# Kernel optimization log

Hardware: AMD Instinct MI355X
Metric: run time of the kernel (lower is better)

## Reference

```python
import jax, jax.numpy as jnp
import numpy as np

N = 100000   # nodes
E = 1600000  # edges
IN, HID, OUT = 128, 128, 64

def setup_inputs() -> dict:
    key = jax.random.key(0)
    ks = jax.random.split(key, 18)
    def lin(k, i, o):
        kw, kb = jax.random.split(k)
        s = 1.0 / np.sqrt(i)
        return (jax.random.uniform(kw, (i, o), jnp.float32, -s, s),
                jax.random.uniform(kb, (o,), jnp.float32, -s, s))
    x = jax.random.normal(ks[0], (N, IN), jnp.float32)
    edge_index = jax.random.randint(ks[1], (2, E), 0, N, jnp.int64)
    W1, b1   = lin(ks[2], IN, HID)
    W21, b21 = lin(ks[3], IN, HID)
    W22, b22 = lin(ks[4], HID, HID)
    W31, b31 = lin(ks[5], IN, HID)
    W32, b32 = lin(ks[6], HID, HID)
    W33, b33 = lin(ks[7], HID, HID)
    Wa, ba   = lin(ks[8], HID, 1)
    Wf, bf   = lin(ks[9], HID, OUT)
    return dict(x=x, edge_index=edge_index, W1=W1, b1=b1, W21=W21, b21=b21,
                W22=W22, b22=b22, W31=W31, b31=b31, W32=W32, b32=b32,
                W33=W33, b33=b33, Wa=Wa, ba=ba, Wf=Wf, bf=bf)

def _gcn(x, W, b, src, dst, dinv):
    # PyG GCNConv: D^{-1/2}(A+I)D^{-1/2} X W + b, self-loops added.
    h = x @ W                                    # [N, F]
    norm = dinv[src] * dinv[dst]                 # [E]
    agg = jax.ops.segment_sum(h[src] * norm[:, None], dst, num_segments=N)
    agg = agg + h * (dinv * dinv)[:, None]       # self-loop contribution
    return agg + b

def reference(x, edge_index, W1, b1, W21, b21, W22, b22, W31, b31,
              W32, b32, W33, b33, Wa, ba, Wf, bf):
    src, dst = edge_index[0], edge_index[1]
    # degree with self-loops (in-degree at target nodes)
    deg = jax.ops.segment_sum(jnp.ones(E, x.dtype), dst, num_segments=N) + 1.0
    dinv = jax.lax.rsqrt(deg)
    h1 = jax.nn.relu(_gcn(x, W1, b1, src, dst, dinv))
    h2 = jax.nn.relu(_gcn(x, W21, b21, src, dst, dinv))
    h2 = jax.nn.relu(_gcn(h2, W22, b22, src, dst, dinv))
    h3 = jax.nn.relu(_gcn(x, W31, b31, src, dst, dinv))
    h3 = jax.nn.relu(_gcn(h3, W32, b32, src, dst, dinv))
    h3 = jax.nn.relu(_gcn(h3, W33, b33, src, dst, dinv))
    H = jnp.stack([h1, h2, h3], axis=1)          # [N, 3, HID]
    scores = H @ Wa + ba                         # [N, 3, 1]
    w = jax.nn.softmax(scores, axis=1)
    h_meta = jnp.sum(w * H, axis=1)              # [N, HID]
    h_out = h_meta + h1
    return h_out @ Wf + bf                       # [N, OUT]
```

## Files before the change

### kernel.cpp

```cpp
#include <hip/hip_runtime.h>
#include <hip/hip_bf16.h>

#define HIDF 128
#define OUTF 64
#define SCAN_B 256

typedef __attribute__((ext_vector_type(8))) short bf16x8;
typedef __attribute__((ext_vector_type(4))) float f32x4;

__device__ __forceinline__ float us2f(unsigned u_lo16) {
    return __uint_as_float(u_lo16 << 16);
}
__device__ __forceinline__ unsigned short f2us(float f) {
    __hip_bfloat16 h = __float2bfloat16(f);
    return *reinterpret_cast<unsigned short*>(&h);
}
__device__ __forceinline__ unsigned pack2(float a, float b) {
    return (unsigned)f2us(a) | ((unsigned)f2us(b) << 16);
}

__global__ __launch_bounds__(256) void deg_zero(int* __restrict__ d, int N) {
    int i = blockIdx.x * 256 + threadIdx.x;
    if (i < N) d[i] = 0;
}

__global__ __launch_bounds__(256) void deg_count(const int* __restrict__ ei, int* __restrict__ d, int E) {
    int e = blockIdx.x * 256 + threadIdx.x;
    if (e < E) atomicAdd(&d[ei[E + e]], 1);
}

__global__ __launch_bounds__(256) void scanA(const int* __restrict__ degi, int* __restrict__ blocksum, int N) {
    __shared__ int red[256];
    const int b = blockIdx.x;
    const int chunk = (N + SCAN_B - 1) / SCAN_B;
    const int lo = b * chunk, hi = min(lo + chunk, N);
    int s = 0;
    for (int i = lo + threadIdx.x; i < hi; i += 256) s += degi[i];
    red[threadIdx.x] = s;
    __syncthreads();
    for (int off = 128; off; off >>= 1) {
        if (threadIdx.x < off) red[threadIdx.x] += red[threadIdx.x + off];
        __syncthreads();
    }
    if (threadIdx.x == 0) blocksum[b] = red[0];
}

__global__ __launch_bounds__(256) void scanB(const int* __restrict__ blocksum, int* __restrict__ blockoff) {
    __shared__ int ps[256];
    const int t = threadIdx.x;
    ps[t] = blocksum[t];
    __syncthreads();
    for (int off = 1; off < 256; off <<= 1) {
        int v = ps[t];
        int u = (t >= off) ? ps[t - off] : 0;
        __syncthreads();
        ps[t] = v + u;
        __syncthreads();
    }
    blockoff[t] = (t == 0) ? 0 : ps[t - 1];
}

__global__ __launch_bounds__(256) void scanC(const int* __restrict__ degi,
                                             const int* __restrict__ blockoff,
                                             int* __restrict__ cursor,
                                             float* __restrict__ dinv, int N) {
    __shared__ int ps[256];
    const int b = blockIdx.x;
    const int chunk = (N + SCAN_B - 1) / SCAN_B;
    const int lo = b * chunk, hi = min(lo + chunk, N);
    const int tchunk = (chunk + 255) / 256;
    const int tlo = lo + threadIdx.x * tchunk;
    const int thi = min(tlo + tchunk, hi);
    int s = 0;
    for (int i = tlo; i < thi; ++i) s += degi[i];
    ps[threadIdx.x] = s;
    __syncthreads();
    for (int off = 1; off < 256; off <<= 1) {
        int v = ps[threadIdx.x];
        int u = (threadIdx.x >= off) ? ps[threadIdx.x - off] : 0;
        __syncthreads();
        ps[threadIdx.x] = v + u;
        __syncthreads();
    }
    int base = blockoff[b] + ((threadIdx.x == 0) ? 0 : ps[threadIdx.x - 1]);
    for (int i = tlo; i < thi; ++i) {
        int d = degi[i];
        cursor[i] = base;
        base += d;
        dinv[i] = rsqrtf((float)d + 1.f);
    }
}

__global__ __launch_bounds__(256) void scatter_kernel(const int* __restrict__ ei,
                                                      int* __restrict__ cursor,
                                                      int* __restrict__ csr_src, int E) {
    int e = blockIdx.x * 256 + threadIdx.x;
    if (e >= E) return;
    int pos = atomicAdd(&cursor[ei[E + e]], 1);
    csr_src[pos] = ei[e];
}

__global__ __launch_bounds__(256) void cvt_scale(const float* __restrict__ X,
                                                 const float* __restrict__ dinv,
                                                 unsigned short* __restrict__ TB, int N) {
    int g = blockIdx.x * 256 + threadIdx.x;
    if (g >= N * 32) return;
    int n = g >> 5;
    float dv = dinv[n];
    float4 v = ((const float4*)X)[g];
    ushort4 o;
    o.x = f2us(v.x * dv); o.y = f2us(v.y * dv);
    o.z = f2us(v.z * dv); o.w = f2us(v.w * dv);
    ((ushort4*)TB)[g] = o;
}

__global__ __launch_bounds__(256) void cvt_w(const float* __restrict__ Wa0,
                                             const float* __restrict__ Wa1,
                                             const float* __restrict__ Wa2,
                                             const float* __restrict__ Wa3,
                                             const float* __restrict__ Wa4,
                                             unsigned short* __restrict__ WTB) {
    int t = blockIdx.x * 256 + threadIdx.x;
    if (t >= 5 * 16384) return;
    int m = t >> 14, local = t & 16383;
    int n = local >> 7, k = local & 127;
    const float* src = (m == 0) ? Wa0 : (m == 1) ? Wa1 : (m == 2) ? Wa2 : (m == 3) ? Wa3 : Wa4;
    WTB[t] = f2us(src[k * 128 + n]);
}

template <bool OUT_BF16>
__global__ __launch_bounds__(256) void agg_b(const unsigned short* __restrict__ TB,
                                             const float* __restrict__ dinv,
                                             const int* __restrict__ csr_src,
                                             const int* __restrict__ rend,
                                             void* __restrict__ O, int N) {
    const int n = (blockIdx.x * 256 + threadIdx.x) >> 6;
    const int lane = threadIdx.x & 63;
    if (n >= N) return;
    const int start = (n == 0) ? 0 : rend[n - 1];
    const int end   = rend[n];
    const unsigned* Tv = (const unsigned*)TB;

    float ax0 = 0.f, ay0 = 0.f, ax1 = 0.f, ay1 = 0.f;
    int e = start;
    for (; e + 8 <= end; e += 8) {
        int s0 = csr_src[e + 0], s1 = csr_src[e + 1], s2 = csr_src[e + 2], s3 = csr_src[e + 3];
        int s4 = csr_src[e + 4], s5 = csr_src[e + 5], s6 = csr_src[e + 6], s7 = csr_src[e + 7];
        unsigned v0 = Tv[(size_t)s0 * 64 + lane];
        unsigned v1 = Tv[(size_t)s1 * 64 + lane];
        unsigned v2 = Tv[(size_t)s2 * 64 + lane];
        unsigned v3 = Tv[(size_t)s3 * 64 + lane];
        unsigned v4 = Tv[(size_t)s4 * 64 + lane];
        unsigned v5 = Tv[(size_t)s5 * 64 + lane];
        unsigned v6 = Tv[(size_t)s6 * 64 + lane];
        unsigned v7 = Tv[(size_t)s7 * 64 + lane];
        ax0 += us2f(v0 & 0xffffu); ay0 += __uint_as_float(v0 & 0xffff0000u);
        ax1 += us2f(v1 & 0xffffu); ay1 += __uint_as_float(v1 & 0xffff0000u);
        ax0 += us2f(v2 & 0xffffu); ay0 += __uint_as_float(v2 & 0xffff0000u);
        ax1 += us2f(v3 & 0xffffu); ay1 += __uint_as_float(v3 & 0xffff0000u);
        ax0 += us2f(v4 & 0xffffu); ay0 += __uint_as_float(v4 & 0xffff0000u);
        ax1 += us2f(v5 & 0xffffu); ay1 += __uint_as_float(v5 & 0xffff0000u);
        ax0 += us2f(v6 & 0xffffu); ay0 += __uint_as_float(v6 & 0xffff0000u);
        ax1 += us2f(v7 & 0xffffu); ay1 += __uint_as_float(v7 & 0xffff0000u);
    }
    if (e + 4 <= end) {
        int s0 = csr_src[e + 0], s1 = csr_src[e + 1], s2 = csr_src[e + 2], s3 = csr_src[e + 3];
        unsigned v0 = Tv[(size_t)s0 * 64 + lane];
        unsigned v1 = Tv[(size_t)s1 * 64 + lane];
        unsigned v2 = Tv[(size_t)s2 * 64 + lane];
        unsigned v3 = Tv[(size_t)s3 * 64 + lane];
        ax0 += us2f(v0 & 0xffffu); ay0 += __uint_as_float(v0 & 0xffff0000u);
        ax1 += us2f(v1 & 0xffffu); ay1 += __uint_as_float(v1 & 0xffff0000u);
        ax0 += us2f(v2 & 0xffffu); ay0 += __uint_as_float(v2 & 0xffff0000u);
        ax1 += us2f(v3 & 0xffffu); ay1 += __uint_as_float(v3 & 0xffff0000u);
        e += 4;
    }
    for (; e < end; ++e) {
        int s = csr_src[e];
        unsigned v = Tv[(size_t)s * 64 + lane];
        ax0 += us2f(v & 0xffffu);
        ay0 += __uint_as_float(v & 0xffff0000u);
    }
    unsigned sv = Tv[(size_t)n * 64 + lane];
    ax0 += us2f(sv & 0xffffu);
    ay0 += __uint_as_float(sv & 0xffff0000u);
    const float dv = dinv[n];
    float ox = (ax0 + ax1) * dv;
    float oy = (ay0 + ay1) * dv;
    if (OUT_BF16) {
        ((unsigned*)O)[(size_t)n * 64 + lane] = pack2(ox, oy);
    } else {
        float2 o; o.x = ox; o.y = oy;
        ((float2*)O)[(size_t)n * 64 + lane] = o;
    }
}

__global__ __launch_bounds__(256) void agg_dual(const unsigned short* __restrict__ TB23,
                                                const float* __restrict__ dinv,
                                                const int* __restrict__ csr_src,
                                                const int* __restrict__ rend,
                                                unsigned* __restrict__ OA,
                                                unsigned* __restrict__ OB, int N) {
    const int n = (blockIdx.x * 256 + threadIdx.x) >> 6;
    const int lane = threadIdx.x & 63;
    if (n >= N) return;
    const int start = (n == 0) ? 0 : rend[n - 1];
    const int end   = rend[n];
    const unsigned* Tv = (const unsigned*)TB23;

    float ax2 = 0.f, ay2 = 0.f, bx2 = 0.f, by2 = 0.f;
    float ax3 = 0.f, ay3 = 0.f, bx3 = 0.f, by3 = 0.f;
    int e = start;
    for (; e + 4 <= end; e += 4) {
        int s0 = csr_src[e + 0], s1 = csr_src[e + 1], s2 = csr_src[e + 2], s3 = csr_src[e + 3];
        unsigned a0 = Tv[(size_t)s0 * 128 + lane];
        unsigned c0 = Tv[(size_t)s0 * 128 + 64 + lane];
        unsigned a1 = Tv[(size_t)s1 * 128 + lane];
        unsigned c1 = Tv[(size_t)s1 * 128 + 64 + lane];
        unsigned a2 = Tv[(size_t)s2 * 128 + lane];
        unsigned c2 = Tv[(size_t)s2 * 128 + 64 + lane];
        unsigned a3 = Tv[(size_t)s3 * 128 + lane];
        unsigned c3 = Tv[(size_t)s3 * 128 + 64 + lane];
        ax2 += us2f(a0 & 0xffffu); ay2 += __uint_as_float(a0 & 0xffff0000u);
        ax3 += us2f(c0 & 0xffffu); ay3 += __uint_as_float(c0 & 0xffff0000u);
        bx2 += us2f(a1 & 0xffffu); by2 += __uint_as_float(a1 & 0xffff0000u);
        bx3 += us2f(c1 & 0xffffu); by3 += __uint_as_float(c1 & 0xffff0000u);
        ax2 += us2f(a2 & 0xffffu); ay2 += __uint_as_float(a2 & 0xffff0000u);
        ax3 += us2f(c2 & 0xffffu); ay3 += __uint_as_float(c2 & 0xffff0000u);
        bx2 += us2f(a3 & 0xffffu); by2 += __uint_as_float(a3 & 0xffff0000u);
        bx3 += us2f(c3 & 0xffffu); by3 += __uint_as_float(c3 & 0xffff0000u);
    }
    for (; e < end; ++e) {
        int s = csr_src[e];
        unsigned a = Tv[(size_t)s * 128 + lane];
        unsigned c = Tv[(size_t)s * 128 + 64 + lane];
        ax2 += us2f(a & 0xffffu); ay2 += __uint_as_float(a & 0xffff0000u);
        ax3 += us2f(c & 0xffffu); ay3 += __uint_as_float(c & 0xffff0000u);
    }
    {
        unsigned a = Tv[(size_t)n * 128 + lane];
        unsigned c = Tv[(size_t)n * 128 + 64 + lane];
        ax2 += us2f(a & 0xffffu); ay2 += __uint_as_float(a & 0xffff0000u);
        ax3 += us2f(c & 0xffffu); ay3 += __uint_as_float(c & 0xffff0000u);
    }
    const float dv = dinv[n];
    OA[(size_t)n * 64 + lane] = pack2((ax2 + bx2) * dv, (ay2 + by2) * dv);
    OB[(size_t)n * 64 + lane] = pack2((ax3 + bx3) * dv, (ay3 + by3) * dv);
}

#define OM_BF16 1
#define OM_BF16_SR 2
template <int OMODE, int OSTRIDE, bool INF32>
__global__ __launch_bounds__(256) void gemm_mfma(const void* __restrict__ Xv,
                                                 const unsigned short* __restrict__ WT,
                                                 const float* __restrict__ bias,
                                                 const float* __restrict__ dinv,
                                                 unsigned short* __restrict__ T, int N) {
    __shared__ unsigned short Xs[64 * 128];
    __shared__ unsigned short Ws[128 * 128];
    const int tid = threadIdx.x;
    const int nb = blockIdx.x * 64;

    for (int c = tid; c < 2048; c += 256) {
        int n = c >> 4, kc = c & 15;
        ((uint4*)Ws)[(n << 4) | (kc ^ (n & 7))] = ((const uint4*)WT)[c];
    }
    for (int c = tid; c < 1024; c += 256) {
        int nl = c >> 4, kc = c & 15;
        int n = nb + nl;
        uint4 v = make_uint4(0u, 0u, 0u, 0u);
        if (n < N) {
            if (INF32) {
                const float4* Xr = (const float4*)((const float*)Xv + (size_t)n * HIDF);
                float4 v0 = Xr[kc * 2], v1 = Xr[kc * 2 + 1];
                v.x = pack2(v0.x, v0.y); v.y = pack2(v0.z, v0.w);
                v.z = pack2(v1.x, v1.y); v.w = pack2(v1.z, v1.w);
            } else {
                v = ((const uint4*)((const unsigned short*)Xv + (size_t)n * HIDF))[kc];
            }
        }
        ((uint4*)Xs)[(nl << 4) | (kc ^ (nl & 7))] = v;
    }
    __syncthreads();

    const int wv   = tid >> 6;
    const int l    = tid & 63;
    const int row  = l & 15;
    const int kgrp = l >> 4;

    bf16x8 afr[4];
    #pragma unroll
    for (int kk = 0; kk < 4; ++kk) {
        int nl = 16 * wv + row;
        int kc = kk * 4 + kgrp;
        afr[kk] = *(const bf16x8*)(Xs + nl * 128 + ((kc ^ (nl & 7)) << 3));
    }

    f32x4 acc[8];
    #pragma unroll
    for (int nt = 0; nt < 8; ++nt) {
        float b = bias[nt * 16 + row];
        acc[nt] = (f32x4){b, b, b, b};
    }

    #pragma unroll
    for (int nt = 0; nt < 8; ++nt) {
        int col = nt * 16 + row;
        #pragma unroll
        for (int kk = 0; kk < 4; ++kk) {
            int kc = kk * 4 + kgrp;
            bf16x8 bfr = *(const bf16x8*)(Ws + col * 128 + ((kc ^ (col & 7)) << 3));
            acc[nt] = __builtin_amdgcn_mfma_f32_16x16x32_bf16(afr[kk], bfr, acc[nt], 0, 0, 0);
        }
    }

    float dv[4];
    if (OMODE == OM_BF16_SR) {
        #pragma unroll
        for (int r = 0; r < 4; ++r) {
            int grow = nb + 16 * wv + kgrp * 4 + r;
            dv[r] = (grow < N) ? dinv[grow] : 0.f;
        }
    }
    #pragma unroll
    for (int nt = 0; nt < 8; ++nt) {
        int gcol = nt * 16 + row;
        #pragma unroll
        for (int r = 0; r < 4; ++r) {
            int grow = nb + 16 * wv + kgrp * 4 + r;
            if (grow < N) {
                float v = acc[nt][r];
                if (OMODE == OM_BF16_SR) v = fmaxf(v, 0.f) * dv[r];
                T[(size_t)grow * OSTRIDE + gcol] = f2us(v);
            }
        }
    }
}

__global__ __launch_bounds__(256) void gemm128f(const float* __restrict__ X,
                                                const float* __restrict__ W,
                                                const float* __restrict__ bias,
                                                float* __restrict__ T, int N) {
    __shared__ float Xsh[HIDF][68];
    const int tid = threadIdx.x;
    const int nb = blockIdx.x * 64;
    {
        const int nloc = tid & 63;
        const int n = nb + nloc;
        const int kq0 = tid >> 6;
        if (n < N) {
            const float4* Xr = (const float4*)(X + (size_t)n * HIDF);
            #pragma unroll
            for (int kq = kq0; kq < 32; kq += 4) {
                float4 v = Xr[kq];
                int k = kq * 4;
                Xsh[k + 0][nloc] = v.x; Xsh[k + 1][nloc] = v.y;
                Xsh[k + 2][nloc] = v.z; Xsh[k + 3][nloc] = v.w;
            }
        } else {
            #pragma unroll
            for (int kq = kq0; kq < 32; kq += 4) {
                int k = kq * 4;
                Xsh[k + 0][nloc] = 0.f; Xsh[k + 1][nloc] = 0.f;
                Xsh[k + 2][nloc] = 0.f; Xsh[k + 3][nloc] = 0.f;
            }
        }
    }
    __syncthreads();

    const int j4  = tid & 31;
    const int sub = tid >> 5;
    const float4* Wrow = (const float4*)W;
    const float4 bv = ((const float4*)bias)[j4];

    float4 acc[8];
    #pragma unroll
    for (int i = 0; i < 8; ++i) acc[i] = bv;

    #pragma unroll 4
    for (int k = 0; k < HIDF; ++k) {
        float4 w = Wrow[k * 32 + j4];
        float xv[8];
        *(float4*)&xv[0] = *(const float4*)&Xsh[k][sub * 8];
        *(float4*)&xv[4] = *(const float4*)&Xsh[k][sub * 8 + 4];
        #pragma unroll
        for (int i = 0; i < 8; ++i) {
            acc[i].x = fmaf(xv[i], w.x, acc[i].x);
            acc[i].y = fmaf(xv[i], w.y, acc[i].y);
            acc[i].z = fmaf(xv[i], w.z, acc[i].z);
            acc[i].w = fmaf(xv[i], w.w, acc[i].w);
        }
    }
    #pragma unroll
    for (int i = 0; i < 8; ++i) {
        int n = nb + sub * 8 + i;
        if (n < N) *((float4*)&T[(size_t)n * HIDF + j4 * 4]) = acc[i];
    }
}

__global__ __launch_bounds__(256) void meta_kernel(const float* __restrict__ H1,
                                                   const unsigned short* __restrict__ H2B,
                                                   const unsigned short* __restrict__ H3B,
                                                   const float* __restrict__ Wa,
                                                   const float* __restrict__ ba,
                                                   const float* __restrict__ Wf,
                                                   const float* __restrict__ bfb,
                                                   float* __restrict__ out, int N) {
    __shared__ float WfS[HIDF * OUTF];
    __shared__ float WaS[HIDF];
    __shared__ float hm[4][HIDF];
    const int tid = threadIdx.x;
    for (int i = tid; i < HIDF * OUTF; i += 256) WfS[i] = Wf[i];
    if (tid < HIDF) WaS[tid] = Wa[tid];
    __syncthreads();
    const float bav = ba[0];
    const int w = tid >> 6;
    const int l = tid & 63;
    const float bfv = bfb[l];
    const int iters = (N + 3) >> 2;

    for (int it = blockIdx.x; it < iters; it += gridDim.x) {
        const int n = it * 4 + w;
        __syncthreads();
        if (n < N) {
            const float* h1 = H1 + (size_t)n * HIDF;
            const unsigned short* h2 = H2B + (size_t)n * HIDF;
            const unsigned short* h3 = H3B + (size_t)n * HIDF;
            float h1a = fmaxf(h1[l], 0.f),       h1b = fmaxf(h1[l + 64], 0.f);
            float h2a = fmaxf(us2f(h2[l]), 0.f), h2b = fmaxf(us2f(h2[l + 64]), 0.f);
            float h3a = fmaxf(us2f(h3[l]), 0.f), h3b = fmaxf(us2f(h3[l + 64]), 0.f);
            float s1 = h1a * WaS[l] + h1b * WaS[l + 64];
            float s2 = h2a * WaS[l] + h2b * WaS[l + 64];
            float s3 = h3a * WaS[l] + h3b * WaS[l + 64];
            #pragma unroll
            for (int off = 32; off; off >>= 1) {
                s1 += __shfl_xor(s1, off);
                s2 += __shfl_xor(s2, off);
                s3 += __shfl_xor(s3, off);
            }
            s1 += bav; s2 += bav; s3 += bav;
            float m  = fmaxf(s1, fmaxf(s2, s3));
            float e1 = expf(s1 - m), e2 = expf(s2 - m), e3 = expf(s3 - m);
            float inv = 1.f / (e1 + e2 + e3);
            float w1 = e1 * inv, w2 = e2 * inv, w3 = e3 * inv;
            hm[w][l]      = w1 * h1a + w2 * h2a + w3 * h3a + h1a;
            hm[w][l + 64] = w1 * h1b + w2 * h2b + w3 * h3b + h1b;
        }
        __syncthreads();
        if (n < N) {
            float acc = bfv;
            #pragma unroll
            for (int k = 0; k < HIDF; ++k) acc = fmaf(hm[w][k], WfS[k * OUTF + l], acc);
            out[(size_t)n * OUTF + l] = acc;
        }
    }
}

extern "C" void kernel_launch(void* const* d_in, const int* in_sizes, int n_in,
                              void* d_out, int out_size, void* d_ws, size_t ws_size,
                              hipStream_t stream) {
    const float* x   = (const float*)d_in[0];
    const int*   ei  = (const int*)d_in[1];
    const float *W1  = (const float*)d_in[2],  *b1  = (const float*)d_in[3];
    const float *W21 = (const float*)d_in[4],  *b21 = (const float*)d_in[5];
    const float *W22 = (const float*)d_in[6],  *b22 = (const float*)d_in[7];
    const float *W31 = (const float*)d_in[8],  *b31 = (const float*)d_in[9];
    const float *W32 = (const float*)d_in[10], *b32 = (const float*)d_in[11];
    const float *W33 = (const float*)d_in[12], *b33 = (const float*)d_in[13];
    const float *Wa  = (const float*)d_in[14], *ba  = (const float*)d_in[15];
    const float *Wf  = (const float*)d_in[16], *bfb = (const float*)d_in[17];

    const int N = in_sizes[0] / HIDF;
    const int E = in_sizes[1] / 2;

    int*   DEGI    = (int*)d_ws;
    int*   CURSOR  = DEGI + N;
    int*   CSR_SRC = CURSOR + N;
    int*   BSUM    = CSR_SRC + E;
    int*   BOFF    = BSUM + 256;
    float* DINV    = (float*)(BOFF + 256);
    unsigned short* TB23 = (unsigned short*)(DINV + N);
    float* PX      = (float*)(TB23 + (size_t)N * 256);
    unsigned* AGA  = (unsigned*)(PX + (size_t)N * HIDF);
    unsigned* AGB  = AGA + (size_t)N * 64;
    unsigned* H2B  = AGB + (size_t)N * 64;
    unsigned short* WTB = (unsigned short*)(H2B + (size_t)N * 64);

    const int gN    = (N + 255) / 256;
    const int gE    = (E + 255) / 256;
    const int gCVT  = (N * 32 + 255) / 256;
    const int gAGG  = (N * 64 + 255) / 256;
    const int gGEMM = (N + 63) / 64;
    const int gMETA = 2048;

    deg_zero<<<gN, 256, 0, stream>>>(DEGI, N);
    deg_count<<<gE, 256, 0, stream>>>(ei, DEGI, E);
    scanA<<<SCAN_B, 256, 0, stream>>>(DEGI, BSUM, N);
    scanB<<<1, 256, 0, stream>>>(BSUM, BOFF);
    scanC<<<SCAN_B, 256, 0, stream>>>(DEGI, BOFF, CURSOR, DINV, N);
    scatter_kernel<<<gE, 256, 0, stream>>>(ei, CURSOR, CSR_SRC, E);
    cvt_w<<<320, 256, 0, stream>>>(W21, W31, W22, W32, W33, WTB);

    unsigned short* TBX = TB23;

    cvt_scale<<<gCVT, 256, 0, stream>>>(x, DINV, TBX, N);
    agg_b<false><<<gAGG, 256, 0, stream>>>(TBX, DINV, CSR_SRC, CURSOR, PX, N);

    gemm_mfma<OM_BF16_SR, 256, true><<<gGEMM, 256, 0, stream>>>(PX, WTB,           b21, DINV, TB23,       N);
    gemm_mfma<OM_BF16_SR, 256, true><<<gGEMM, 256, 0, stream>>>(PX, WTB + 16384,   b31, DINV, TB23 + 128, N);
    agg_dual<<<gAGG, 256, 0, stream>>>(TB23, DINV, CSR_SRC, CURSOR, AGA, AGB, N);

    gemm_mfma<OM_BF16, 128, false><<<gGEMM, 256, 0, stream>>>(AGA, WTB + 2 * 16384, b22, DINV, (unsigned short*)H2B, N);
    gemm_mfma<OM_BF16_SR, 128, false><<<gGEMM, 256, 0, stream>>>(AGB, WTB + 3 * 16384, b32, DINV, TBX, N);
    agg_b<true><<<gAGG, 256, 0, stream>>>(TBX, DINV, CSR_SRC, CURSOR, AGA, N);
    gemm_mfma<OM_BF16, 128, false><<<gGEMM, 256, 0, stream>>>(AGA, WTB + 4 * 16384, b33, DINV, (unsigned short*)AGB, N);

    gemm128f<<<gGEMM, 256, 0, stream>>>(PX, W1, b1, PX, N);

    meta_kernel<<<gMETA, 256, 0, stream>>>(PX, (const unsigned short*)H2B,
                                           (const unsigned short*)AGB, Wa, ba, Wf, bfb,
                                           (float*)d_out, N);
}
```

Before: 752.5 us.

## Bucket CSR scatter, store first aggregation in bf16, and run h1 GEMM on MFMA

The CSR build now scatters edges into 128-node buckets first and then does a per-destination scatter. This is meant to improve locality for the atomic cursor updates and the csr_src writes. The first aggregation (A·x) is stored as bf16 instead of fp32, which halves its write traffic and the GEMM read traffic. The fp32 FMA gemm128f for layer 1 is replaced by the bf16 MFMA GEMM with an fp32 output. In exchange there is an extra pass over an int2 edge buffer and reduced precision in the h1 path.

```diff
diff --git a/kernel.cpp b/kernel.cpp
--- a/kernel.cpp
+++ b/kernel.cpp
@@ -4,6 +4,7 @@
 #define HIDF 128
 #define OUTF 64
 #define SCAN_B 256
+#define BK_SHIFT 7
 
 typedef __attribute__((ext_vector_type(8))) short bf16x8;
 typedef __attribute__((ext_vector_type(4))) float f32x4;
@@ -91,13 +92,31 @@
     }
 }
 
-__global__ __launch_bounds__(256) void scatter_kernel(const int* __restrict__ ei,
-                                                      int* __restrict__ cursor,
-                                                      int* __restrict__ csr_src, int E) {
+__global__ __launch_bounds__(256) void bcur_init(const int* __restrict__ cursor,
+                                                 int* __restrict__ bcur, int N, int NBK) {
+    int b = blockIdx.x * 256 + threadIdx.x;
+    if (b < NBK) bcur[b * 64] = cursor[b << BK_SHIFT];
+}
+
+__global__ __launch_bounds__(256) void bucket_scatter(const int* __restrict__ ei,
+                                                      int* __restrict__ bcur,
+                                                      int2* __restrict__ edg, int E) {
     int e = blockIdx.x * 256 + threadIdx.x;
     if (e >= E) return;
-    int pos = atomicAdd(&cursor[ei[E + e]], 1);
-    csr_src[pos] = ei[e];
+    int src = ei[e];
+    int dst = ei[E + e];
+    int pos = atomicAdd(&bcur[(dst >> BK_SHIFT) * 64], 1);
+    edg[pos] = make_int2(src, dst);
+}
+
+__global__ __launch_bounds__(256) void final_scatter(const int2* __restrict__ edg,
+                                                     int* __restrict__ cursor,
+                                                     int* __restrict__ csr_src, int E) {
+    int p = blockIdx.x * 256 + threadIdx.x;
+    if (p >= E) return;
+    int2 sd = edg[p];
+    int pos = atomicAdd(&cursor[sd.y], 1);
+    csr_src[pos] = sd.x;
 }
 
 __global__ __launch_bounds__(256) void cvt_scale(const float* __restrict__ X,
@@ -119,12 +138,14 @@
                                              const float* __restrict__ Wa2,
                                              const float* __restrict__ Wa3,
                                              const float* __restrict__ Wa4,
+                                             const float* __restrict__ Wa5,
                                              unsigned short* __restrict__ WTB) {
     int t = blockIdx.x * 256 + threadIdx.x;
-    if (t >= 5 * 16384) return;
+    if (t >= 6 * 16384) return;
     int m = t >> 14, local = t & 16383;
     int n = local >> 7, k = local & 127;
-    const float* src = (m == 0) ? Wa0 : (m == 1) ? Wa1 : (m == 2) ? Wa2 : (m == 3) ? Wa3 : Wa4;
+    const float* src = (m == 0) ? Wa0 : (m == 1) ? Wa1 : (m == 2) ? Wa2
+                     : (m == 3) ? Wa3 : (m == 4) ? Wa4 : Wa5;
     WTB[t] = f2us(src[k * 128 + n]);
 }
 
@@ -248,14 +269,15 @@
     OB[(size_t)n * 64 + lane] = pack2((ax3 + bx3) * dv, (ay3 + by3) * dv);
 }
 
+#define OM_F32 0
 #define OM_BF16 1
 #define OM_BF16_SR 2
-template <int OMODE, int OSTRIDE, bool INF32>
-__global__ __launch_bounds__(256) void gemm_mfma(const void* __restrict__ Xv,
+template <int OMODE, int OSTRIDE>
+__global__ __launch_bounds__(256) void gemm_mfma(const unsigned short* __restrict__ Xb,
                                                  const unsigned short* __restrict__ WT,
                                                  const float* __restrict__ bias,
                                                  const float* __restrict__ dinv,
-                                                 unsigned short* __restrict__ T, int N) {
+                                                 void* __restrict__ T, int N) {
     __shared__ unsigned short Xs[64 * 128];
     __shared__ unsigned short Ws[128 * 128];
     const int tid = threadIdx.x;
@@ -269,16 +291,7 @@
         int nl = c >> 4, kc = c & 15;
         int n = nb + nl;
         uint4 v = make_uint4(0u, 0u, 0u, 0u);
-        if (n < N) {
-            if (INF32) {
-                const float4* Xr = (const float4*)((const float*)Xv + (size_t)n * HIDF);
-                float4 v0 = Xr[kc * 2], v1 = Xr[kc * 2 + 1];
-                v.x = pack2(v0.x, v0.y); v.y = pack2(v0.z, v0.w);
-                v.z = pack2(v1.x, v1.y); v.w = pack2(v1.z, v1.w);
-            } else {
-                v = ((const uint4*)((const unsigned short*)Xv + (size_t)n * HIDF))[kc];
-            }
-        }
+        if (n < N) v = ((const uint4*)(Xb + (size_t)n * HIDF))[kc];
         ((uint4*)Xs)[(nl << 4) | (kc ^ (nl & 7))] = v;
     }
     __syncthreads();
@@ -331,70 +344,13 @@
             if (grow < N) {
                 float v = acc[nt][r];
                 if (OMODE == OM_BF16_SR) v = fmaxf(v, 0.f) * dv[r];
-                T[(size_t)grow * OSTRIDE + gcol] = f2us(v);
+                if (OMODE == OM_F32) {
+                    ((float*)T)[(size_t)grow * OSTRIDE + gcol] = v;
+                } else {
+                    ((unsigned short*)T)[(size_t)grow * OSTRIDE + gcol] = f2us(v);
+                }
             }
         }
-    }
-}
-
-__global__ __launch_bounds__(256) void gemm128f(const float* __restrict__ X,
-                                                const float* __restrict__ W,
-                                                const float* __restrict__ bias,
-                                                float* __restrict__ T, int N) {
-    __shared__ float Xsh[HIDF][68];
-    const int tid = threadIdx.x;
-    const int nb = blockIdx.x * 64;
-    {
-        const int nloc = tid & 63;
-        const int n = nb + nloc;
-        const int kq0 = tid >> 6;
-        if (n < N) {
-            const float4* Xr = (const float4*)(X + (size_t)n * HIDF);
-            #pragma unroll
-            for (int kq = kq0; kq < 32; kq += 4) {
-                float4 v = Xr[kq];
-                int k = kq * 4;
-                Xsh[k + 0][nloc] = v.x; Xsh[k + 1][nloc] = v.y;
-                Xsh[k + 2][nloc] = v.z; Xsh[k + 3][nloc] = v.w;
-            }
-        } else {
-            #pragma unroll
-            for (int kq = kq0; kq < 32; kq += 4) {
-                int k = kq * 4;
-                Xsh[k + 0][nloc] = 0.f; Xsh[k + 1][nloc] = 0.f;
-                Xsh[k + 2][nloc] = 0.f; Xsh[k + 3][nloc] = 0.f;
-            }
-        }
-    }
-    __syncthreads();
-
-    const int j4  = tid & 31;
-    const int sub = tid >> 5;
-    const float4* Wrow = (const float4*)W;
-    const float4 bv = ((const float4*)bias)[j4];
-
-    float4 acc[8];
-    #pragma unroll
-    for (int i = 0; i < 8; ++i) acc[i] = bv;
-
-    #pragma unroll 4
-    for (int k = 0; k < HIDF; ++k) {
-        float4 w = Wrow[k * 32 + j4];
-        float xv[8];
-        *(float4*)&xv[0] = *(const float4*)&Xsh[k][sub * 8];
-        *(float4*)&xv[4] = *(const float4*)&Xsh[k][sub * 8 + 4];
-        #pragma unroll
-        for (int i = 0; i < 8; ++i) {
-            acc[i].x = fmaf(xv[i], w.x, acc[i].x);
-            acc[i].y = fmaf(xv[i], w.y, acc[i].y);
-            acc[i].z = fmaf(xv[i], w.z, acc[i].z);
-            acc[i].w = fmaf(xv[i], w.w, acc[i].w);
-        }
-    }
-    #pragma unroll
-    for (int i = 0; i < 8; ++i) {
-        int n = nb + sub * 8 + i;
-        if (n < N) *((float4*)&T[(size_t)n * HIDF + j4 * 4]) = acc[i];
     }
 }
 
@@ -472,16 +428,19 @@
 
     const int N = in_sizes[0] / HIDF;
     const int E = in_sizes[1] / 2;
+    const int NBK = (N + 127) >> BK_SHIFT;
 
     int*   DEGI    = (int*)d_ws;
     int*   CURSOR  = DEGI + N;
     int*   CSR_SRC = CURSOR + N;
-    int*   BSUM    = CSR_SRC + E;
+    int2*  EDG     = (int2*)(CSR_SRC + E);
+    int*   BCUR    = (int*)(EDG + E);
+    int*   BSUM    = BCUR + 1024 * 64;
     int*   BOFF    = BSUM + 256;
     float* DINV    = (float*)(BOFF + 256);
     unsigned short* TB23 = (unsigned short*)(DINV + N);
-    float* PX      = (float*)(TB23 + (size_t)N * 256);
-    unsigned* AGA  = (unsigned*)(PX + (size_t)N * HIDF);
+    unsigned* PXB  = (unsigned*)(TB23 + (size_t)N * 256);
+    unsigned* AGA  = PXB + (size_t)N * 64;
     unsigned* AGB  = AGA + (size_t)N * 64;
     unsigned* H2B  = AGB + (size_t)N * 64;
     unsigned short* WTB = (unsigned short*)(H2B + (size_t)N * 64);
@@ -498,26 +457,29 @@
     scanA<<<SCAN_B, 256, 0, stream>>>(DEGI, BSUM, N);
     scanB<<<1, 256, 0, stream>>>(BSUM, BOFF);
     scanC<<<SCAN_B, 256, 0, stream>>>(DEGI, BOFF, CURSOR, DINV, N);
-    scatter_kernel<<<gE, 256, 0, stream>>>(ei, CURSOR, CSR_SRC, E);
-    cvt_w<<<320, 256, 0, stream>>>(W21, W31, W22, W32, W33, WTB);
+    bcur_init<<<(NBK + 255) / 256, 256, 0, stream>>>(CURSOR, BCUR, N, NBK);
+    bucket_scatter<<<gE, 256, 0, stream>>>(ei, BCUR, EDG, E);
+    final_scatter<<<gE, 256, 0, stream>>>(EDG, CURSOR, CSR_SRC, E);
+    cvt_w<<<384, 256, 0, stream>>>(W21, W31, W22, W32, W33, W1, WTB);
 
     unsigned short* TBX = TB23;
 
     cvt_scale<<<gCVT, 256, 0, stream>>>(x, DINV, TBX, N);
-    agg_b<false><<<gAGG, 256, 0, stream>>>(TBX, DINV, CSR_SRC, CURSOR, PX, N);
-
-    gemm_mfma<OM_BF16_SR, 256, true><<<gGEMM, 256, 0, stream>>>(PX, WTB,           b21, DINV, TB23,       N);
-    gemm_mfma<OM_BF16_SR, 256, true><<<gGEMM, 256, 0, stream>>>(PX, WTB + 16384,   b31, DINV, TB23 + 128, N);
+    agg_b<true><<<gAGG, 256, 0, stream>>>(TBX, DINV, CSR_SRC, CURSOR, PXB, N);
+
+    gemm_mfma<OM_BF16_SR, 256><<<gGEMM, 256, 0, stream>>>((unsigned short*)PXB, WTB,         b21, DINV, TB23,       N);
+    gemm_mfma<OM_BF16_SR, 256><<<gGEMM, 256, 0, stream>>>((unsigned short*)PXB, WTB + 16384, b31, DINV, TB23 + 128, N);
     agg_dual<<<gAGG, 256, 0, stream>>>(TB23, DINV, CSR_SRC, CURSOR, AGA, AGB, N);
 
-    gemm_mfma<OM_BF16, 128, false><<<gGEMM, 256, 0, stream>>>(AGA, WTB + 2 * 16384, b22, DINV, (unsigned short*)H2B, N);
-    gemm_mfma<OM_BF16_SR, 128, false><<<gGEMM, 256, 0, stream>>>(AGB, WTB + 3 * 16384, b32, DINV, TBX, N);
+    gemm_mfma<OM_BF16, 128><<<gGEMM, 256, 0, stream>>>((unsigned short*)AGA, WTB + 2 * 16384, b22, DINV, H2B, N);
+    gemm_mfma<OM_BF16_SR, 128><<<gGEMM, 256, 0, stream>>>((unsigned short*)AGB, WTB + 3 * 16384, b32, DINV, TBX, N);
     agg_b<true><<<gAGG, 256, 0, stream>>>(TBX, DINV, CSR_SRC, CURSOR, AGA, N);
-    gemm_mfma<OM_BF16, 128, false><<<gGEMM, 256, 0, stream>>>(AGA, WTB + 4 * 16384, b33, DINV, (unsigned short*)AGB, N);
-
-    gemm128f<<<gGEMM, 256, 0, stream>>>(PX, W1, b1, PX, N);
-
-    meta_kernel<<<gMETA, 256, 0, stream>>>(PX, (const unsigned short*)H2B,
+    gemm_mfma<OM_BF16, 128><<<gGEMM, 256, 0, stream>>>((unsigned short*)AGA, WTB + 4 * 16384, b33, DINV, AGB, N);
+
+    float* H1F = (float*)TB23;
+    gemm_mfma<OM_F32, 128><<<gGEMM, 256, 0, stream>>>((unsigned short*)PXB, WTB + 5 * 16384, b1, DINV, H1F, N);
+
+    meta_kernel<<<gMETA, 256, 0, stream>>>(H1F, (const unsigned short*)H2B,
                                            (const unsigned short*)AGB, Wa, ba, Wf, bfb,
                                            (float*)d_out, N);
 }
```

New measurement: 726.6 us. 3.4% less time.
